# Performance work log

Hardware: AMD Instinct MI355X
Metric: run time of the kernel (lower is better)

The kernel has to match this reference:

```python
import jax, jax.numpy as jnp
import numpy as np

N = 11616          # IMDB total nodes (hard-coded slices in source)
NHID = 512
L = 4              # num_layers (encoder and decoder each)
E = 371712         # ~32 avg degree
SIZES = [4278, 2081, 5257]
FEATS = [3066, 2081, 5257]
GAMMA = 3.0


def setup_inputs() -> dict:
    key = jax.random.key(0)
    ks = jax.random.split(key, 24)
    s = 0.02
    d = {}
    d["X0"] = jax.random.normal(ks[0], (SIZES[0], FEATS[0]), jnp.float32)
    d["X1"] = jax.random.normal(ks[1], (SIZES[1], FEATS[1]), jnp.float32)
    d["X2"] = jax.random.normal(ks[2], (SIZES[2], FEATS[2]), jnp.float32)
    d["src"] = jax.random.randint(ks[3], (E,), 0, N)
    d["dst"] = jax.random.randint(ks[4], (E,), 0, N)
    d["edge_w"] = jax.random.uniform(ks[5], (E,), jnp.float32) / 32.0  # ~normalized adjacency values
    d["adj_full"] = (jax.random.uniform(ks[6], (N, N), jnp.float32) < 0.005).astype(jnp.float32)
    # input projections fc_list: feat_dim -> nhid
    for i in range(3):
        d[f"fc_W{i}"] = jax.random.normal(ks[7 + i], (FEATS[i], NHID), jnp.float32) * s
        d[f"fc_b{i}"] = jnp.zeros((NHID,), jnp.float32)
    # stacked GraphConvolution weights (encoder / decoder)
    d["enc_W"] = jax.random.normal(ks[10], (L, NHID, NHID), jnp.float32) * s
    d["enc_b"] = jnp.zeros((L, NHID), jnp.float32)
    d["dec_W"] = jax.random.normal(ks[11], (L, NHID, NHID), jnp.float32) * s
    d["dec_b"] = jnp.zeros((L, NHID), jnp.float32)
    # output projections fc_list2: nhid -> feat_dim
    for i in range(3):
        d[f"out_W{i}"] = jax.random.normal(ks[12 + i], (NHID, FEATS[i]), jnp.float32) * s
        d[f"out_b{i}"] = jnp.zeros((FEATS[i],), jnp.float32)
    return d


def reference(X0, X1, X2, edge_w, adj_full,
              fc_W0, fc_b0, fc_W1, fc_b1, fc_W2, fc_b2,
              enc_W, enc_b, dec_W, dec_b,
              out_W0, out_b0, out_W1, out_b1, out_W2, out_b2,
              src, dst):
    def spmm(h):  # sparse A @ h via edge list
        return jax.ops.segment_sum(h[src] * edge_w[:, None], dst, num_segments=N)

    # per-type input projection, concat over node types -> [N, NHID]
    x = jnp.concatenate([X0 @ fc_W0 + fc_b0,
                         X1 @ fc_W1 + fc_b1,
                         X2 @ fc_W2 + fc_b2], axis=0)

    # encoder then decoder; per source: relu+dropout only at layer 0 (L>1 branch),
    # residual add for layers i>0; dropout is identity in eval mode.
    for W, b in ((enc_W, enc_b), (dec_W, dec_b)):
        for i in range(L):
            h = spmm(x @ W[i]) + b[i]
            x = jax.nn.relu(h) if i == 0 else x + h

    # IMDB slices of final embedding
    e0, e1, e2 = x[:SIZES[0]], x[SIZES[0]:SIZES[0] + SIZES[1]], x[SIZES[0] + SIZES[1]:]
    r0 = e0 @ out_W0 + out_b0
    r1 = e1 @ out_W1 + out_b1
    r2 = e2 @ out_W2 + out_b2

    # emb_loss_fun2: BCE(sigmoid(x x^T), adj_full), mean. Stable form:
    z = x @ x.T  # [N, N]
    emb_loss = jnp.mean(adj_full * jax.nn.softplus(-z) + (1.0 - adj_full) * jax.nn.softplus(z))

    # recon_loss_fun2 on type-0 features (cosine-based, power gamma)
    rn = r0 / jnp.maximum(jnp.linalg.norm(r0, axis=-1, keepdims=True), 1e-12)
    fn = X0 / jnp.maximum(jnp.linalg.norm(X0, axis=1, keepdims=True), 1e-12)
    recon_loss = jnp.mean((1.0 - jnp.sum(rn * fn, axis=-1)) ** GAMMA)

    return (r0, r1, r2, emb_loss, recon_loss)
```

## Files before the change

kernel.cpp:

```cpp
#include <hip/hip_runtime.h>
#include <math.h>

#define N_NODES 11616
#define NROWPAD 11776
#define NHID    512
#define EDGES   371712
#define S0 4278
#define S1 2081
#define S2 5257
#define F0 3066
#define F1 2081
#define F2 5257
#define NB2 46
#define NZB2 1081
#define FC_KS 4
#define WPR 363

typedef __attribute__((ext_vector_type(8))) short bf16x8;
typedef __attribute__((ext_vector_type(4))) float f32x4;

#define GL2LDS(g, l) __builtin_amdgcn_global_load_lds(                         \
    (const __attribute__((address_space(1))) unsigned int*)(g),                \
    (__attribute__((address_space(3))) unsigned int*)(l), 16, 0, 0)

__device__ __forceinline__ int slot_of(int row, int kg)
{
    return row * 4 + (kg ^ ((row >> 1) & 3));
}

__device__ __forceinline__ float bf2f(short s)
{
    return __uint_as_float(((unsigned)(unsigned short)s) << 16);
}

__global__ void k_init(double* __restrict__ accum, int* __restrict__ indeg,
                       int* __restrict__ cursor)
{
    int i = blockIdx.x * blockDim.x + threadIdx.x;
    if (i < 2) accum[i] = 0.0;
    if (i < N_NODES) { indeg[i] = 0; cursor[i] = 0; }
}

__global__ void k_padzero(short* __restrict__ xh, short* __restrict__ xl)
{
    int i = blockIdx.x * blockDim.x + threadIdx.x;
    const int base  = N_NODES * NHID;
    const int total = (NROWPAD - N_NODES) * NHID;
    if (i < total) { xh[base + i] = 0; xl[base + i] = 0; }
}

__global__ void k_adjbits(const float* __restrict__ adj, unsigned* __restrict__ bits)
{
    const long i = (long)blockIdx.x * 256 + threadIdx.x;
    const long total = (long)N_NODES * WPR;
    if (i >= total) return;
    const int r = (int)(i / WPR);
    const int w = (int)(i % WPR);
    const float4* rp = reinterpret_cast<const float4*>(adj + (long)r * N_NODES + w * 32);
    unsigned m = 0;
    #pragma unroll
    for (int j4 = 0; j4 < 8; ++j4) {
        float4 v = rp[j4];
        int b = j4 * 4;
        m |= (v.x != 0.f) ? (1u << b)       : 0u;
        m |= (v.y != 0.f) ? (1u << (b + 1)) : 0u;
        m |= (v.z != 0.f) ? (1u << (b + 2)) : 0u;
        m |= (v.w != 0.f) ? (1u << (b + 3)) : 0u;
    }
    bits[i] = m;
}

__global__ void k_count(const int* __restrict__ dst, int* __restrict__ indeg)
{
    int e = blockIdx.x * blockDim.x + threadIdx.x;
    if (e < EDGES) atomicAdd(&indeg[dst[e]], 1);
}

__global__ void k_scan(const int* __restrict__ indeg, int* __restrict__ rowptr)
{
    __shared__ int part[256];
    const int t = threadIdx.x;
    const int chunk = (N_NODES + 255) / 256;
    const int base = t * chunk;
    int s = 0;
    for (int i = 0; i < chunk; ++i) {
        int idx = base + i;
        if (idx < N_NODES) s += indeg[idx];
    }
    part[t] = s;
    __syncthreads();
    if (t == 0) for (int i = 1; i < 256; ++i) part[i] += part[i - 1];
    __syncthreads();
    int run = (t == 0) ? 0 : part[t - 1];
    for (int i = 0; i < chunk; ++i) {
        int idx = base + i;
        if (idx < N_NODES) { rowptr[idx] = run; run += indeg[idx]; }
    }
    if (t == 0) rowptr[N_NODES] = part[255];
}

__global__ void k_fill(const int* __restrict__ src, const int* __restrict__ dst,
                       const float* __restrict__ ew, const int* __restrict__ rowptr,
                       int* __restrict__ cursor, int* __restrict__ csrc,
                       float* __restrict__ cw)
{
    int e = blockIdx.x * blockDim.x + threadIdx.x;
    if (e >= EDGES) return;
    int d = dst[e];
    int pos = rowptr[d] + atomicAdd(&cursor[d], 1);
    csrc[pos] = src[e];
    cw[pos]   = ew[e];
}

__device__ __forceinline__ void split_bf16(float f, short& hi, short& lo)
{
    unsigned u  = __float_as_uint(f);
    unsigned hr = (u + 0x7FFFu + ((u >> 16) & 1u)) & 0xFFFF0000u;
    float    fh = __uint_as_float(hr);
    float    fl = f - fh;
    unsigned ul = __float_as_uint(fl);
    unsigned lr = ul + 0x7FFFu + ((ul >> 16) & 1u);
    hi = (short)(hr >> 16);
    lo = (short)(lr >> 16);
}

__global__ void k_splitpad(const float* __restrict__ in, short* __restrict__ oh,
                           short* __restrict__ ol, int R, int C, int Cpad)
{
    const int c = blockIdx.x * 256 + threadIdx.x;
    const int r = blockIdx.y;
    if (c >= Cpad) return;
    float f = (r < R && c < C) ? in[(long)r * C + c] : 0.f;
    short h, l;
    split_bf16(f, h, l);
    oh[(long)r * Cpad + c] = h;
    ol[(long)r * Cpad + c] = l;
}

__global__ void k_tsplit(const float* __restrict__ in, short* __restrict__ oh,
                         short* __restrict__ ol, int R, int C, int Rpad, int Cpad)
{
    __shared__ float tile[32][33];
    const int cb = blockIdx.x * 32, rb = blockIdx.y * 32;
    const int tx = threadIdx.x, ty = threadIdx.y;
    #pragma unroll
    for (int i = ty; i < 32; i += 8) {
        int r = rb + i, c = cb + tx;
        tile[i][tx] = (r < R && c < C) ? in[(long)r * C + c] : 0.f;
    }
    __syncthreads();
    #pragma unroll
    for (int i = ty; i < 32; i += 8) {
        int row = cb + i, col = rb + tx;
        if (row < Cpad && col < Rpad) {
            short h, l;
            split_bf16(tile[tx][i], h, l);
            oh[(long)row * Rpad + col] = h;
            ol[(long)row * Rpad + col] = l;
        }
    }
}

__device__ __forceinline__ void stage_gl(const short* __restrict__ src, int ldk,
                                         int k0, short* ldsPanel, int lane)
{
    #pragma unroll
    for (int i = 0; i < 8; ++i) {
        int ci  = i * 64 + lane;
        int row = ci >> 2;
        int kgs = (ci & 3) ^ ((row >> 1) & 3);
        const short* g = src + (long)row * ldk + k0 + kgs * 8;
        GL2LDS(g, (char*)ldsPanel + i * 1024);
    }
}

__device__ __forceinline__ void stage_gl256(const short* __restrict__ src, int ldk,
                                            int k0, short* ldsPanel, int half, int lane)
{
    #pragma unroll
    for (int i = 0; i < 8; ++i) {
        int ci  = i * 128 + half * 64 + lane;
        int row = ci >> 2;
        int kgs = (ci & 3) ^ ((row >> 1) & 3);
        const short* g = src + (long)row * ldk + k0 + kgs * 8;
        GL2LDS(g, (char*)ldsPanel + i * 2048 + half * 1024);
    }
}

__global__ __launch_bounds__(256, 3)
void k_gemm_bb(const short* __restrict__ Agh, const short* __restrict__ Agl,
               const short* __restrict__ Bgh, const short* __restrict__ Bgl,
               const float* __restrict__ bias, float* __restrict__ C,
               int M, int NN, int Kpad, int ldk)
{
    __shared__ short P[4][4096];
    const int t = threadIdx.x, lane = t & 63, w = t >> 6;
    const int rowBase = blockIdx.y * 128, colBase = blockIdx.x * 128;
    const int wm = (w >> 1) * 64, wn = (w & 1) * 64;
    const int kg = lane >> 4, fr = lane & 15;

    const short* srcs[4] = { Agh + (long)rowBase * ldk, Agl + (long)rowBase * ldk,
                             Bgh + (long)colBase * ldk, Bgl + (long)colBase * ldk };
    const short* mySrc = srcs[w];

    int offA[4], offB[4];
    #pragma unroll
    for (int f = 0; f < 4; ++f) {
        int rA = wm + f * 16 + fr, rB = wn + f * 16 + fr;
        offA[f] = slot_of(rA, kg) * 8;
        offB[f] = slot_of(rB, kg) * 8;
    }

    f32x4 acc[4][4];
    #pragma unroll
    for (int i = 0; i < 4; ++i)
        #pragma unroll
        for (int j = 0; j < 4; ++j)
            acc[i][j] = (f32x4){0.f, 0.f, 0.f, 0.f};

    for (int k0 = 0; k0 < Kpad; k0 += 32) {
        stage_gl(mySrc, ldk, k0, &P[w][0], lane);
        __syncthreads();
        bf16x8 ah[4], al[4], bh[4], bl[4];
        #pragma unroll
        for (int f = 0; f < 4; ++f) {
            ah[f] = *(const bf16x8*)&P[0][offA[f]];
            al[f] = *(const bf16x8*)&P[1][offA[f]];
            bh[f] = *(const bf16x8*)&P[2][offB[f]];
            bl[f] = *(const bf16x8*)&P[3][offB[f]];
        }
        #pragma unroll
        for (int i = 0; i < 4; ++i)
            #pragma unroll
            for (int j = 0; j < 4; ++j) {
                acc[i][j] = __builtin_amdgcn_mfma_f32_16x16x32_bf16(ah[i], bh[j], acc[i][j], 0, 0, 0);
                acc[i][j] = __builtin_amdgcn_mfma_f32_16x16x32_bf16(ah[i], bl[j], acc[i][j], 0, 0, 0);
                acc[i][j] = __builtin_amdgcn_mfma_f32_16x16x32_bf16(al[i], bh[j], acc[i][j], 0, 0, 0);
            }
        __syncthreads();
    }

    #pragma unroll
    for (int i = 0; i < 4; ++i) {
        #pragma unroll
        for (int q = 0; q < 4; ++q) {
            int r = rowBase + wm + i * 16 + kg * 4 + q;
            if (r >= M) continue;
            #pragma unroll
            for (int j = 0; j < 4; ++j) {
                int c = colBase + wn + j * 16 + fr;
                if (c < NN)
                    C[(long)r * NN + c] = acc[i][j][q] + (bias ? bias[c] : 0.f);
            }
        }
    }
}

__global__ __launch_bounds__(512, 2)
void k_gemm_bb2(const short* __restrict__ Agh, const short* __restrict__ Agl,
                const short* __restrict__ Bgh, const short* __restrict__ Bgl,
                const float* __restrict__ bias, float* __restrict__ C,
                int M, int NN, int Kpad, int ldk)
{
    __shared__ short P[4][8192];
    const int t = threadIdx.x, lane = t & 63, w = t >> 6;
    const int rowBase = blockIdx.y * 256, colBase = blockIdx.x * 256;
    const int kg = lane >> 4, fr = lane & 15;
    const int half = w & 1;
    const int wr = w >> 2, wc = w & 3;

    const short* srcs[4] = { Agh + (long)rowBase * ldk, Agl + (long)rowBase * ldk,
                             Bgh + (long)colBase * ldk, Bgl + (long)colBase * ldk };
    const short* mySrc = srcs[w >> 1];

    int offA[8], offB[4];
    #pragma unroll
    for (int i = 0; i < 8; ++i) offA[i] = slot_of(wr * 128 + i * 16 + fr, kg) * 8;
    #pragma unroll
    for (int j = 0; j < 4; ++j) offB[j] = slot_of(wc * 64 + j * 16 + fr, kg) * 8;

    f32x4 acc[8][4];
    #pragma unroll
    for (int i = 0; i < 8; ++i)
        #pragma unroll
        for (int j = 0; j < 4; ++j)
            acc[i][j] = (f32x4){0.f, 0.f, 0.f, 0.f};

    for (int k0 = 0; k0 < Kpad; k0 += 32) {
        stage_gl256(mySrc, ldk, k0, &P[w >> 1][0], half, lane);
        __syncthreads();
        bf16x8 bh[4], bl[4];
        #pragma unroll
        for (int j = 0; j < 4; ++j) {
            bh[j] = *(const bf16x8*)&P[2][offB[j]];
            bl[j] = *(const bf16x8*)&P[3][offB[j]];
        }
        #pragma unroll
        for (int i = 0; i < 8; ++i) {
            bf16x8 ah = *(const bf16x8*)&P[0][offA[i]];
            bf16x8 al = *(const bf16x8*)&P[1][offA[i]];
            #pragma unroll
            for (int j = 0; j < 4; ++j) {
                acc[i][j] = __builtin_amdgcn_mfma_f32_16x16x32_bf16(ah, bh[j], acc[i][j], 0, 0, 0);
                acc[i][j] = __builtin_amdgcn_mfma_f32_16x16x32_bf16(ah, bl[j], acc[i][j], 0, 0, 0);
                acc[i][j] = __builtin_amdgcn_mfma_f32_16x16x32_bf16(al, bh[j], acc[i][j], 0, 0, 0);
            }
        }
        __syncthreads();
    }

    #pragma unroll
    for (int i = 0; i < 8; ++i) {
        #pragma unroll
        for (int q = 0; q < 4; ++q) {
            int r = rowBase + wr * 128 + i * 16 + kg * 4 + q;
            if (r >= M) continue;
            #pragma unroll
            for (int j = 0; j < 4; ++j) {
                int c = colBase + wc * 64 + j * 16 + fr;
                if (c < NN)
                    C[(long)r * NN + c] = acc[i][j][q] + bias[c];
            }
        }
    }
}

__global__ __launch_bounds__(256, 3)
void k_gemm_red(const short* __restrict__ Agh, const short* __restrict__ Agl,
                const short* __restrict__ Bgh, const short* __restrict__ Bgl,
                float* __restrict__ Cpart, int M, int ldk, int kChunk)
{
    __shared__ short P[4][4096];
    const int t = threadIdx.x, lane = t & 63, w = t >> 6;
    const int rowBase = blockIdx.y * 128, colBase = blockIdx.x * 128;
    const int z = blockIdx.z;
    const int wm = (w >> 1) * 64, wn = (w & 1) * 64;
    const int kg = lane >> 4, fr = lane & 15;

    const short* srcs[4] = { Agh + (long)rowBase * ldk, Agl + (long)rowBase * ldk,
                             Bgh + (long)colBase * ldk, Bgl + (long)colBase * ldk };
    const short* mySrc = srcs[w];

    int offA[4], offB[4];
    #pragma unroll
    for (int f = 0; f < 4; ++f) {
        int rA = wm + f * 16 + fr, rB = wn + f * 16 + fr;
        offA[f] = slot_of(rA, kg) * 8;
        offB[f] = slot_of(rB, kg) * 8;
    }

    f32x4 acc[4][4];
    #pragma unroll
    for (int i = 0; i < 4; ++i)
        #pragma unroll
        for (int j = 0; j < 4; ++j)
            acc[i][j] = (f32x4){0.f, 0.f, 0.f, 0.f};

    const int kEnd = z * kChunk + kChunk;
    for (int k0 = z * kChunk; k0 < kEnd; k0 += 32) {
        stage_gl(mySrc, ldk, k0, &P[w][0], lane);
        __syncthreads();
        bf16x8 ah[4], al[4], bh[4], bl[4];
        #pragma unroll
        for (int f = 0; f < 4; ++f) {
            ah[f] = *(const bf16x8*)&P[0][offA[f]];
            al[f] = *(const bf16x8*)&P[1][offA[f]];
            bh[f] = *(const bf16x8*)&P[2][offB[f]];
            bl[f] = *(const bf16x8*)&P[3][offB[f]];
        }
        #pragma unroll
        for (int i = 0; i < 4; ++i)
            #pragma unroll
            for (int j = 0; j < 4; ++j) {
                acc[i][j] = __builtin_amdgcn_mfma_f32_16x16x32_bf16(ah[i], bh[j], acc[i][j], 0, 0, 0);
                acc[i][j] = __builtin_amdgcn_mfma_f32_16x16x32_bf16(ah[i], bl[j], acc[i][j], 0, 0, 0);
                acc[i][j] = __builtin_amdgcn_mfma_f32_16x16x32_bf16(al[i], bh[j], acc[i][j], 0, 0, 0);
            }
        __syncthreads();
    }

    #pragma unroll
    for (int i = 0; i < 4; ++i) {
        #pragma unroll
        for (int q = 0; q < 4; ++q) {
            int r = rowBase + wm + i * 16 + kg * 4 + q;
            if (r >= M) continue;
            #pragma unroll
            for (int j = 0; j < 4; ++j) {
                int c = colBase + wn + j * 16 + fr;
                Cpart[((long)z * M + r) * NHID + c] = acc[i][j][q];
            }
        }
    }
}

__global__ void k_fcreduce(const float* __restrict__ Cpart, const float* __restrict__ bias,
                           int M, short* __restrict__ oh, short* __restrict__ ol)
{
    const int r = blockIdx.x;
    const int c = threadIdx.x << 2;
    float4 s = *reinterpret_cast<const float4*>(bias + c);
    #pragma unroll
    for (int z = 0; z < FC_KS; ++z) {
        const float4 p = *reinterpret_cast<const float4*>(Cpart + ((long)z * M + r) * NHID + c);
        s.x += p.x; s.y += p.y; s.z += p.z; s.w += p.w;
    }
    short4 h, l;
    split_bf16(s.x, h.x, l.x); split_bf16(s.y, h.y, l.y);
    split_bf16(s.z, h.z, l.z); split_bf16(s.w, h.w, l.w);
    *reinterpret_cast<short4*>(oh + (long)r * NHID + c) = h;
    *reinterpret_cast<short4*>(ol + (long)r * NHID + c) = l;
}

__global__ __launch_bounds__(512, 2)
void k_zloss(const short* __restrict__ xh, const short* __restrict__ xl,
             const unsigned* __restrict__ bits, double* __restrict__ accum)
{
    __shared__ short P[4][8192];
    __shared__ float ztr[8][16][17];
    __shared__ float red[512];
    const int t = threadIdx.x, lane = t & 63, w = t >> 6;

    int L;
    {
        const int q = NZB2 / 8, rr = NZB2 % 8;
        int xcd = blockIdx.x & 7, pos = blockIdx.x >> 3;
        L = (xcd < rr) ? xcd * (q + 1) + pos : rr * (q + 1) + (xcd - rr) * q + pos;
    }
    int R = 0;
    while (L >= NB2 - R) { L -= NB2 - R; ++R; }
    const int Cb = R + L;
    const int rowBase = R * 256, colBase = Cb * 256;
    const int diag = (Cb == R);

    const int kg = lane >> 4, fr = lane & 15;
    const int half = w & 1;
    const int wr = w >> 2, wc = w & 3;

    const short* srcs[4] = { xh + (long)rowBase * NHID, xl + (long)rowBase * NHID,
                             xh + (long)colBase * NHID, xl + (long)colBase * NHID };
    const short* mySrc = srcs[w >> 1];

    int offA[8], offB[4];
    #pragma unroll
    for (int i = 0; i < 8; ++i) offA[i] = slot_of(wr * 128 + i * 16 + fr, kg) * 8;
    #pragma unroll
    for (int j = 0; j < 4; ++j) offB[j] = slot_of(wc * 64 + j * 16 + fr, kg) * 8;

    f32x4 acc[8][4];
    #pragma unroll
    for (int i = 0; i < 8; ++i)
        #pragma unroll
        for (int j = 0; j < 4; ++j)
            acc[i][j] = (f32x4){0.f, 0.f, 0.f, 0.f};

    for (int k0 = 0; k0 < NHID; k0 += 32) {
        stage_gl256(mySrc, NHID, k0, &P[w >> 1][0], half, lane);
        __syncthreads();
        bf16x8 bh[4], bl[4];
        #pragma unroll
        for (int j = 0; j < 4; ++j) {
            bh[j] = *(const bf16x8*)&P[2][offB[j]];
            bl[j] = *(const bf16x8*)&P[3][offB[j]];
        }
        #pragma unroll
        for (int i = 0; i < 8; ++i) {
            bf16x8 ah = *(const bf16x8*)&P[0][offA[i]];
            bf16x8 al = *(const bf16x8*)&P[1][offA[i]];
            #pragma unroll
            for (int j = 0; j < 4; ++j) {
                acc[i][j] = __builtin_amdgcn_mfma_f32_16x16x32_bf16(ah, bh[j], acc[i][j], 0, 0, 0);
                acc[i][j] = __builtin_amdgcn_mfma_f32_16x16x32_bf16(ah, bl[j], acc[i][j], 0, 0, 0);
                acc[i][j] = __builtin_amdgcn_mfma_f32_16x16x32_bf16(al, bh[j], acc[i][j], 0, 0, 0);
            }
        }
        __syncthreads();
    }

    float local = 0.f;
    #pragma unroll
    for (int i = 0; i < 8; ++i) {
        #pragma unroll
        for (int q = 0; q < 4; ++q) {
            int r = rowBase + wr * 128 + i * 16 + kg * 4 + q;
            if (r >= N_NODES) continue;
            #pragma unroll
            for (int j = 0; j < 4; ++j) {
                int c = colBase + wc * 64 + j * 16 + fr;
                if (c >= N_NODES) continue;
                float z  = acc[i][j][q];
                float sp = fmaxf(z, 0.f) + __logf(1.f + __expf(-fabsf(z)));
                unsigned wd = bits[(long)r * WPR + (c >> 5)];
                float az = ((wd >> (c & 31)) & 1u) ? z : 0.f;
                local += diag ? (sp - az) : (2.f * sp - az);
            }
        }
    }
    if (!diag) {
        #pragma unroll
        for (int i = 0; i < 8; ++i) {
            #pragma unroll
            for (int j = 0; j < 4; ++j) {
                #pragma unroll
                for (int q = 0; q < 4; ++q)
                    ztr[w][kg * 4 + q][fr] = acc[i][j][q];
                #pragma unroll
                for (int q = 0; q < 4; ++q) {
                    float zt = ztr[w][fr][kg * 4 + q];
                    int cc = colBase + wc * 64 + j * 16 + kg * 4 + q;
                    int rr = rowBase + wr * 128 + i * 16 + fr;
                    if (cc < N_NODES && rr < N_NODES) {
                        unsigned wd = bits[(long)cc * WPR + (rr >> 5)];
                        if ((wd >> (rr & 31)) & 1u) local -= zt;
                    }
                }
            }
        }
    }
    red[t] = local;
    __syncthreads();
    for (int sft = 256; sft > 0; sft >>= 1) {
        if (t < sft) red[t] += red[t + sft];
        __syncthreads();
    }
    if (t == 0) atomicAdd(accum, (double)red[0]);
}

__global__ void k_spmm(const float* __restrict__ y,
                       const int* __restrict__ rowptr, const int* __restrict__ csrc,
                       const float* __restrict__ cw, const float* __restrict__ bias,
                       int do_relu, short* __restrict__ xh, short* __restrict__ xl)
{
    const int wv   = threadIdx.x >> 6;
    const int lane = threadIdx.x & 63;
    const int n    = blockIdx.x * 2 + (wv >> 1);
    const int c    = (wv & 1) * 256 + (lane << 2);
    float4 s = make_float4(0.f, 0.f, 0.f, 0.f);
    const int beg = rowptr[n], end = rowptr[n + 1];
    for (int e = beg; e < end; ++e) {
        int   sn = csrc[e];
        float wt = cw[e];
        const float4 yv = *reinterpret_cast<const float4*>(y + (long)sn * NHID + c);
        s.x = fmaf(wt, yv.x, s.x);
        s.y = fmaf(wt, yv.y, s.y);
        s.z = fmaf(wt, yv.z, s.z);
        s.w = fmaf(wt, yv.w, s.w);
    }
    const float4 bv = *reinterpret_cast<const float4*>(bias + c);
    float4 o;
    o.x = s.x + bv.x; o.y = s.y + bv.y; o.z = s.z + bv.z; o.w = s.w + bv.w;
    if (do_relu) {
        o.x = fmaxf(o.x, 0.f); o.y = fmaxf(o.y, 0.f);
        o.z = fmaxf(o.z, 0.f); o.w = fmaxf(o.w, 0.f);
    } else {
        const short4 h4 = *reinterpret_cast<const short4*>(xh + (long)n * NHID + c);
        const short4 l4 = *reinterpret_cast<const short4*>(xl + (long)n * NHID + c);
        o.x += bf2f(h4.x) + bf2f(l4.x);
        o.y += bf2f(h4.y) + bf2f(l4.y);
        o.z += bf2f(h4.z) + bf2f(l4.z);
        o.w += bf2f(h4.w) + bf2f(l4.w);
    }
    short4 h, l;
    split_bf16(o.x, h.x, l.x); split_bf16(o.y, h.y, l.y);
    split_bf16(o.z, h.z, l.z); split_bf16(o.w, h.w, l.w);
    *reinterpret_cast<short4*>(xh + (long)n * NHID + c) = h;
    *reinterpret_cast<short4*>(xl + (long)n * NHID + c) = l;
}

__global__ void k_recon(const float* __restrict__ r0, const float* __restrict__ X0,
                        double* __restrict__ accum)
{
    const int row = blockIdx.x;
    const int t = threadIdx.x;
    float dot = 0.f, nr = 0.f, nf = 0.f;
    for (int c = t; c < F0; c += 256) {
        float a = r0[(long)row * F0 + c];
        float b = X0[(long)row * F0 + c];
        dot = fmaf(a, b, dot);
        nr  = fmaf(a, a, nr);
        nf  = fmaf(b, b, nf);
    }
    #pragma unroll
    for (int o = 32; o > 0; o >>= 1) {
        dot += __shfl_down(dot, o);
        nr  += __shfl_down(nr, o);
        nf  += __shfl_down(nf, o);
    }
    __shared__ float sd[3][4];
    const int lane = t & 63, wid = t >> 6;
    if (lane == 0) { sd[0][wid] = dot; sd[1][wid] = nr; sd[2][wid] = nf; }
    __syncthreads();
    if (t == 0) {
        float d = sd[0][0] + sd[0][1] + sd[0][2] + sd[0][3];
        float a = sd[1][0] + sd[1][1] + sd[1][2] + sd[1][3];
        float b = sd[2][0] + sd[2][1] + sd[2][2] + sd[2][3];
        float cosv = d / (fmaxf(sqrtf(a), 1e-12f) * fmaxf(sqrtf(b), 1e-12f));
        float v = 1.f - cosv;
        atomicAdd(accum + 1, (double)(v * v * v));
    }
}

__global__ void k_final(const double* __restrict__ accum, float* __restrict__ out)
{
    if (threadIdx.x == 0) {
        out[45082958] = (float)(accum[0] / ((double)N_NODES * (double)N_NODES));
        out[45082959] = (float)(accum[1] / (double)S0);
    }
}

extern "C" void kernel_launch(void* const* d_in, const int* in_sizes, int n_in,
                              void* d_out, int out_size, void* d_ws, size_t ws_size,
                              hipStream_t stream)
{
    const float* X0  = (const float*)d_in[0];
    const float* X1  = (const float*)d_in[1];
    const float* X2  = (const float*)d_in[2];
    const int*   src = (const int*)d_in[3];
    const int*   dst = (const int*)d_in[4];
    const float* ew  = (const float*)d_in[5];
    const float* adj = (const float*)d_in[6];
    const float* fcW[3]  = {(const float*)d_in[7],  (const float*)d_in[9],  (const float*)d_in[11]};
    const float* fcB[3]  = {(const float*)d_in[8],  (const float*)d_in[10], (const float*)d_in[12]};
    const float* encW = (const float*)d_in[13];
    const float* encB = (const float*)d_in[14];
    const float* decW = (const float*)d_in[15];
    const float* decB = (const float*)d_in[16];
    const float* outW[3] = {(const float*)d_in[17], (const float*)d_in[19], (const float*)d_in[21]};
    const float* outB[3] = {(const float*)d_in[18], (const float*)d_in[20], (const float*)d_in[22]};
    float* out = (float*)d_out;

    const int FD[3]     = {F0, F1, F2};
    const int FPAD[3]   = {(F0 + 127) & ~127, (F1 + 127) & ~127, (F2 + 127) & ~127};
    const int SPAD[3]   = {(S0 + 127) & ~127, (S1 + 127) & ~127, (S2 + 127) & ~127};
    const int FDP2[3]   = {(F0 + 255) & ~255, (F1 + 255) & ~255, (F2 + 255) & ~255};
    const int SD[3]     = {S0, S1, S2};
    const float* XD[3]  = {X0, X1, X2};

    char* ws = (char*)d_ws;
    size_t off = 0;
    auto alloc = [&](size_t bytes) { void* p = ws + off; off += (bytes + 255) & ~(size_t)255; return p; };

    double* accum = (double*)alloc(16);
    const size_t XB = (size_t)N_NODES * NHID * sizeof(float);
    float* ybuf = (float*)alloc(XB);
    float* xalt = (float*)alloc(XB);
    short* xh   = (short*)alloc((size_t)NROWPAD * NHID * 2);
    short* xl   = (short*)alloc((size_t)NROWPAD * NHID * 2);
    const size_t XSmax = (size_t)5376 * 5376;
    short* Xsh  = (short*)alloc(XSmax * 2);
    short* Xsl  = (short*)alloc(XSmax * 2);
    short* fcWh = (short*)alloc((size_t)NHID * 5376 * 2);
    short* fcWl = (short*)alloc((size_t)NHID * 5376 * 2);
    short* wTh  = (short*)alloc((size_t)8 * NHID * NHID * 2);
    short* wTl  = (short*)alloc((size_t)8 * NHID * NHID * 2);
    unsigned* bits = (unsigned*)alloc((size_t)N_NODES * WPR * 4);
    int* indeg  = (int*)alloc((size_t)N_NODES * 4);
    int* rowptr = (int*)alloc((size_t)(N_NODES + 1) * 4);
    int* cursor = (int*)alloc((size_t)N_NODES * 4);
    int* csrc   = (int*)alloc((size_t)EDGES * 4);
    float* cw   = (float*)alloc((size_t)EDGES * 4);

    float* cpart = ybuf;

    k_init<<<dim3((N_NODES + 255) / 256), dim3(256), 0, stream>>>(accum, indeg, cursor);
    k_padzero<<<dim3(((NROWPAD - N_NODES) * NHID + 255) / 256), dim3(256), 0, stream>>>(xh, xl);
    k_count<<<dim3((EDGES + 255) / 256), dim3(256), 0, stream>>>(dst, indeg);
    k_scan<<<dim3(1), dim3(256), 0, stream>>>(indeg, rowptr);
    k_fill<<<dim3((EDGES + 255) / 256), dim3(256), 0, stream>>>(src, dst, ew, rowptr, cursor, csrc, cw);
    {
        long words = (long)N_NODES * WPR;
        k_adjbits<<<dim3((unsigned)((words + 255) / 256)), dim3(256), 0, stream>>>(adj, bits);
    }

    auto tgrid = [](int Cpad, int Rpad) { return dim3((unsigned)((Cpad + 31) / 32), (unsigned)((Rpad + 31) / 32)); };
    auto ggrid = [](int m, int nn) { return dim3((unsigned)((nn + 127) / 128), (unsigned)((m + 127) / 128)); };
    auto ggrid2 = [](int m, int nn) { return dim3((unsigned)((nn + 255) / 256), (unsigned)((m + 255) / 256)); };

    for (int i = 0; i < 4; ++i) {
        k_tsplit<<<tgrid(NHID, NHID), dim3(32, 8), 0, stream>>>(
            encW + (size_t)i * NHID * NHID, wTh + (size_t)i * NHID * NHID,
            wTl + (size_t)i * NHID * NHID, NHID, NHID, NHID, NHID);
        k_tsplit<<<tgrid(NHID, NHID), dim3(32, 8), 0, stream>>>(
            decW + (size_t)i * NHID * NHID, wTh + (size_t)(4 + i) * NHID * NHID,
            wTl + (size_t)(4 + i) * NHID * NHID, NHID, NHID, NHID, NHID);
    }

    {
        size_t rowoff = 0;
        for (int i = 0; i < 3; ++i) {
            k_splitpad<<<dim3((FPAD[i] + 255) / 256, SPAD[i]), dim3(256), 0, stream>>>(
                XD[i], Xsh, Xsl, SD[i], FD[i], FPAD[i]);
            k_tsplit<<<tgrid(NHID, FPAD[i]), dim3(32, 8), 0, stream>>>(
                fcW[i], fcWh, fcWl, FD[i], NHID, FPAD[i], NHID);
            k_gemm_red<<<dim3(NHID / 128, SPAD[i] / 128, FC_KS), dim3(256), 0, stream>>>(
                Xsh, Xsl, fcWh, fcWl, cpart, SD[i], FPAD[i], FPAD[i] / FC_KS);
            k_fcreduce<<<dim3(SD[i]), dim3(128), 0, stream>>>(
                cpart, fcB[i], SD[i], xh + rowoff * NHID, xl + rowoff * NHID);
            rowoff += SD[i];
        }
    }

    for (int phase = 0; phase < 2; ++phase) {
        const float* B = phase ? decB : encB;
        for (int i = 0; i < 4; ++i) {
            k_gemm_bb<<<ggrid(N_NODES, NHID), dim3(256), 0, stream>>>(
                xh, xl, wTh + (size_t)(phase * 4 + i) * NHID * NHID,
                wTl + (size_t)(phase * 4 + i) * NHID * NHID,
                nullptr, ybuf, N_NODES, NHID, NHID, NHID);
            k_spmm<<<dim3(N_NODES / 2), dim3(256), 0, stream>>>(
                ybuf, rowptr, csrc, cw, B + (size_t)i * NHID, (i == 0) ? 1 : 0,
                xh, xl);
        }
    }

    short* oWh = Xsh;
    short* oWl = Xsl;
    {
        short *ph = oWh, *pl = oWl;
        for (int i = 0; i < 3; ++i) {
            k_tsplit<<<tgrid(FDP2[i], NHID), dim3(32, 8), 0, stream>>>(
                outW[i], ph, pl, NHID, FD[i], NHID, FDP2[i]);
            ph += (size_t)FDP2[i] * NHID; pl += (size_t)FDP2[i] * NHID;
        }
    }

    {
        short *ph = oWh, *pl = oWl;
        float* oo = out;
        size_t rowoff = 0;
        for (int i = 0; i < 3; ++i) {
            k_gemm_bb2<<<ggrid2(SD[i], FD[i]), dim3(512), 0, stream>>>(
                xh + rowoff * NHID, xl + rowoff * NHID, ph, pl, outB[i], oo,
                SD[i], FD[i], NHID, NHID);
            ph += (size_t)FDP2[i] * NHID; pl += (size_t)FDP2[i] * NHID;
            oo += (size_t)SD[i] * FD[i];
            rowoff += SD[i];
        }
    }

    k_zloss<<<dim3(NZB2), dim3(512), 0, stream>>>(xh, xl, bits, accum);
    k_recon<<<dim3(S0), dim3(256), 0, stream>>>(out, X0, accum);
    k_final<<<dim3(1), dim3(64), 0, stream>>>(accum, out);
}
```

Before: 2.482 ms.

## Use 128-tile GEMM for output projections and alias zloss shared memory

The output-projection GEMMs go back from the 256x256, 512-thread kernel to the existing 128x128, 256-thread k_gemm_bb, with weight padding shrunk to multiples of 128. In k_zloss, the epilogue scratch arrays now share one union with the staging buffers, plus an extra barrier before reuse. This lowers LDS per block, which may allow more resident blocks, but smaller output tiles reload the inputs more often.

```diff
diff --git a/kernel.cpp b/kernel.cpp
--- a/kernel.cpp
+++ b/kernel.cpp
@@ -256,75 +256,6 @@
     }
 }
 
-__global__ __launch_bounds__(512, 2)
-void k_gemm_bb2(const short* __restrict__ Agh, const short* __restrict__ Agl,
-                const short* __restrict__ Bgh, const short* __restrict__ Bgl,
-                const float* __restrict__ bias, float* __restrict__ C,
-                int M, int NN, int Kpad, int ldk)
-{
-    __shared__ short P[4][8192];
-    const int t = threadIdx.x, lane = t & 63, w = t >> 6;
-    const int rowBase = blockIdx.y * 256, colBase = blockIdx.x * 256;
-    const int kg = lane >> 4, fr = lane & 15;
-    const int half = w & 1;
-    const int wr = w >> 2, wc = w & 3;
-
-    const short* srcs[4] = { Agh + (long)rowBase * ldk, Agl + (long)rowBase * ldk,
-                             Bgh + (long)colBase * ldk, Bgl + (long)colBase * ldk };
-    const short* mySrc = srcs[w >> 1];
-
-    int offA[8], offB[4];
-    #pragma unroll
-    for (int i = 0; i < 8; ++i) offA[i] = slot_of(wr * 128 + i * 16 + fr, kg) * 8;
-    #pragma unroll
-    for (int j = 0; j < 4; ++j) offB[j] = slot_of(wc * 64 + j * 16 + fr, kg) * 8;
-
-    f32x4 acc[8][4];
-    #pragma unroll
-    for (int i = 0; i < 8; ++i)
-        #pragma unroll
-        for (int j = 0; j < 4; ++j)
-            acc[i][j] = (f32x4){0.f, 0.f, 0.f, 0.f};
-
-    for (int k0 = 0; k0 < Kpad; k0 += 32) {
-        stage_gl256(mySrc, ldk, k0, &P[w >> 1][0], half, lane);
-        __syncthreads();
-        bf16x8 bh[4], bl[4];
-        #pragma unroll
-        for (int j = 0; j < 4; ++j) {
-            bh[j] = *(const bf16x8*)&P[2][offB[j]];
-            bl[j] = *(const bf16x8*)&P[3][offB[j]];
-        }
-        #pragma unroll
-        for (int i = 0; i < 8; ++i) {
-            bf16x8 ah = *(const bf16x8*)&P[0][offA[i]];
-            bf16x8 al = *(const bf16x8*)&P[1][offA[i]];
-            #pragma unroll
-            for (int j = 0; j < 4; ++j) {
-                acc[i][j] = __builtin_amdgcn_mfma_f32_16x16x32_bf16(ah, bh[j], acc[i][j], 0, 0, 0);
-                acc[i][j] = __builtin_amdgcn_mfma_f32_16x16x32_bf16(ah, bl[j], acc[i][j], 0, 0, 0);
-                acc[i][j] = __builtin_amdgcn_mfma_f32_16x16x32_bf16(al, bh[j], acc[i][j], 0, 0, 0);
-            }
-        }
-        __syncthreads();
-    }
-
-    #pragma unroll
-    for (int i = 0; i < 8; ++i) {
-        #pragma unroll
-        for (int q = 0; q < 4; ++q) {
-            int r = rowBase + wr * 128 + i * 16 + kg * 4 + q;
-            if (r >= M) continue;
-            #pragma unroll
-            for (int j = 0; j < 4; ++j) {
-                int c = colBase + wc * 64 + j * 16 + fr;
-                if (c < NN)
-                    C[(long)r * NN + c] = acc[i][j][q] + bias[c];
-            }
-        }
-    }
-}
-
 __global__ __launch_bounds__(256, 3)
 void k_gemm_red(const short* __restrict__ Agh, const short* __restrict__ Agl,
                 const short* __restrict__ Bgh, const short* __restrict__ Bgl,
@@ -416,9 +347,10 @@
 void k_zloss(const short* __restrict__ xh, const short* __restrict__ xl,
              const unsigned* __restrict__ bits, double* __restrict__ accum)
 {
-    __shared__ short P[4][8192];
-    __shared__ float ztr[8][16][17];
-    __shared__ float red[512];
+    __shared__ union {
+        short P[4][8192];
+        struct { float ztr[8][16][17]; float red[512]; } e;
+    } U;
     const int t = threadIdx.x, lane = t & 63, w = t >> 6;
 
     int L;
@@ -455,18 +387,18 @@
             acc[i][j] = (f32x4){0.f, 0.f, 0.f, 0.f};
 
     for (int k0 = 0; k0 < NHID; k0 += 32) {
-        stage_gl256(mySrc, NHID, k0, &P[w >> 1][0], half, lane);
+        stage_gl256(mySrc, NHID, k0, &U.P[w >> 1][0], half, lane);
         __syncthreads();
         bf16x8 bh[4], bl[4];
         #pragma unroll
         for (int j = 0; j < 4; ++j) {
-            bh[j] = *(const bf16x8*)&P[2][offB[j]];
-            bl[j] = *(const bf16x8*)&P[3][offB[j]];
+            bh[j] = *(const bf16x8*)&U.P[2][offB[j]];
+            bl[j] = *(const bf16x8*)&U.P[3][offB[j]];
         }
         #pragma unroll
         for (int i = 0; i < 8; ++i) {
-            bf16x8 ah = *(const bf16x8*)&P[0][offA[i]];
-            bf16x8 al = *(const bf16x8*)&P[1][offA[i]];
+            bf16x8 ah = *(const bf16x8*)&U.P[0][offA[i]];
+            bf16x8 al = *(const bf16x8*)&U.P[1][offA[i]];
             #pragma unroll
             for (int j = 0; j < 4; ++j) {
                 acc[i][j] = __builtin_amdgcn_mfma_f32_16x16x32_bf16(ah, bh[j], acc[i][j], 0, 0, 0);
@@ -503,10 +435,10 @@
             for (int j = 0; j < 4; ++j) {
                 #pragma unroll
                 for (int q = 0; q < 4; ++q)
-                    ztr[w][kg * 4 + q][fr] = acc[i][j][q];
+                    U.e.ztr[w][kg * 4 + q][fr] = acc[i][j][q];
                 #pragma unroll
                 for (int q = 0; q < 4; ++q) {
-                    float zt = ztr[w][fr][kg * 4 + q];
+                    float zt = U.e.ztr[w][fr][kg * 4 + q];
                     int cc = colBase + wc * 64 + j * 16 + kg * 4 + q;
                     int rr = rowBase + wr * 128 + i * 16 + fr;
                     if (cc < N_NODES && rr < N_NODES) {
@@ -517,13 +449,14 @@
             }
         }
     }
-    red[t] = local;
+    __syncthreads();
+    U.e.red[t] = local;
     __syncthreads();
     for (int sft = 256; sft > 0; sft >>= 1) {
-        if (t < sft) red[t] += red[t + sft];
+        if (t < sft) U.e.red[t] += U.e.red[t + sft];
         __syncthreads();
     }
-    if (t == 0) atomicAdd(accum, (double)red[0]);
+    if (t == 0) atomicAdd(accum, (double)U.e.red[0]);
 }
 
 __global__ void k_spmm(const float* __restrict__ y,
@@ -632,7 +565,6 @@
     const int FD[3]     = {F0, F1, F2};
     const int FPAD[3]   = {(F0 + 127) & ~127, (F1 + 127) & ~127, (F2 + 127) & ~127};
     const int SPAD[3]   = {(S0 + 127) & ~127, (S1 + 127) & ~127, (S2 + 127) & ~127};
-    const int FDP2[3]   = {(F0 + 255) & ~255, (F1 + 255) & ~255, (F2 + 255) & ~255};
     const int SD[3]     = {S0, S1, S2};
     const float* XD[3]  = {X0, X1, X2};
 
@@ -674,7 +606,6 @@
 
     auto tgrid = [](int Cpad, int Rpad) { return dim3((unsigned)((Cpad + 31) / 32), (unsigned)((Rpad + 31) / 32)); };
     auto ggrid = [](int m, int nn) { return dim3((unsigned)((nn + 127) / 128), (unsigned)((m + 127) / 128)); };
-    auto ggrid2 = [](int m, int nn) { return dim3((unsigned)((nn + 255) / 256), (unsigned)((m + 255) / 256)); };
 
     for (int i = 0; i < 4; ++i) {
         k_tsplit<<<tgrid(NHID, NHID), dim3(32, 8), 0, stream>>>(
@@ -718,9 +649,10 @@
     {
         short *ph = oWh, *pl = oWl;
         for (int i = 0; i < 3; ++i) {
-            k_tsplit<<<tgrid(FDP2[i], NHID), dim3(32, 8), 0, stream>>>(
-                outW[i], ph, pl, NHID, FD[i], NHID, FDP2[i]);
-            ph += (size_t)FDP2[i] * NHID; pl += (size_t)FDP2[i] * NHID;
+            int FDP = (FD[i] + 127) & ~127;
+            k_tsplit<<<tgrid(FDP, NHID), dim3(32, 8), 0, stream>>>(
+                outW[i], ph, pl, NHID, FD[i], NHID, FDP);
+            ph += (size_t)FDP * NHID; pl += (size_t)FDP * NHID;
         }
     }
 
@@ -729,10 +661,11 @@
         float* oo = out;
         size_t rowoff = 0;
         for (int i = 0; i < 3; ++i) {
-            k_gemm_bb2<<<ggrid2(SD[i], FD[i]), dim3(512), 0, stream>>>(
+            int FDP = (FD[i] + 127) & ~127;
+            k_gemm_bb<<<ggrid(SD[i], FD[i]), dim3(256), 0, stream>>>(
                 xh + rowoff * NHID, xl + rowoff * NHID, ph, pl, outB[i], oo,
                 SD[i], FD[i], NHID, NHID);
-            ph += (size_t)FDP2[i] * NHID; pl += (size_t)FDP2[i] * NHID;
+            ph += (size_t)FDP * NHID; pl += (size_t)FDP * NHID;
             oo += (size_t)SD[i] * FD[i];
             rowoff += SD[i];
         }
```

Measured after the change: 2.545 ms. +2.5%, slower.
